# Performance work log

Measured on AMD Instinct MI355X. Metric: run time of the kernel, lower is better.

The kernel has to match this reference:

```python
import jax, jax.numpy as jnp
import numpy as np

B, T, N, D = 4, 128, 512, 32
CHEB_K, EMB, HEADS, TA_LAYERS, GCN_NUM, TCN_BLOCKS, KSIZE = 3, 10, 2, 2, 3, 3, 3


def setup_inputs() -> dict:
    key = jax.random.key(0)
    ks = jax.random.split(key, 12)
    x = jax.random.normal(ks[0], (B, T, N, D), jnp.float32)
    init_state = jnp.zeros((1, B, N, D), jnp.float32)  # unused by forward, kept for signature fidelity
    node_embeddings = jax.random.normal(ks[1], (N, EMB), jnp.float32)
    a = jax.random.uniform(ks[2], (N, N), jnp.float32)
    a = 0.5 * (a + a.T)
    adj = a / jnp.sum(a, axis=1, keepdims=True)  # row-normalized dense adjacency
    s = 0.05
    gcn_w = jax.random.normal(ks[3], (GCN_NUM, EMB, CHEB_K, D, D), jnp.float32) * s
    gcn_b = jax.random.normal(ks[4], (GCN_NUM, EMB, D), jnp.float32) * s
    tcn_w1 = jax.random.normal(ks[5], (TCN_BLOCKS, D, D, KSIZE), jnp.float32) * s
    tcn_b1 = jnp.zeros((TCN_BLOCKS, D), jnp.float32)
    tcn_w2 = jax.random.normal(ks[6], (TCN_BLOCKS, D, D, KSIZE), jnp.float32) * s
    tcn_b2 = jnp.zeros((TCN_BLOCKS, D), jnp.float32)
    ta_wq = jax.random.normal(ks[7], (TA_LAYERS, D, D), jnp.float32) * s
    ta_wk = jax.random.normal(ks[8], (TA_LAYERS, D, D), jnp.float32) * s
    ta_wv = jax.random.normal(ks[9], (TA_LAYERS, D, D), jnp.float32) * s
    ta_wo = jax.random.normal(ks[10], (TA_LAYERS, D, D), jnp.float32) * s
    ta_g = jnp.ones((TA_LAYERS, D), jnp.float32)
    ta_b = jnp.zeros((TA_LAYERS, D), jnp.float32)
    return dict(x=x, init_state=init_state, node_embeddings=node_embeddings, adj=adj,
                gcn_w=gcn_w, gcn_b=gcn_b, tcn_w1=tcn_w1, tcn_b1=tcn_b1, tcn_w2=tcn_w2,
                tcn_b2=tcn_b2, ta_wq=ta_wq, ta_wk=ta_wk, ta_wv=ta_wv, ta_wo=ta_wo,
                ta_g=ta_g, ta_b=ta_b)


def _cheb_supports(adj, k):
    I = jnp.eye(adj.shape[0], dtype=adj.dtype)
    s = [I, adj]
    for _ in range(2, k):
        s.append(2.0 * (adj @ s[-1]) - s[-2])
    return jnp.stack(s[:k])  # (k, N, N)


def _emb_gcn(h, supports, E, wp, bp):
    # h: (B,T,N,C); supports: (k,N,N); E: (N,EMB); wp: (EMB,k,C,O); bp: (EMB,O)
    xg = jnp.einsum('knm,btmc->btknc', supports, h)
    W = jnp.einsum('ne,ekco->nkco', E, wp)       # per-node Chebyshev weights
    bias = E @ bp                                 # (N,O)
    return jnp.einsum('btknc,nkco->btno', xg, W) + bias


def _causal_conv(y, w, b, dil):
    # y: (BN, C, T); w: (O, C, K)
    pad = (w.shape[-1] - 1) * dil
    out = jax.lax.conv_general_dilated(y, w, (1,), [(pad, 0)], rhs_dilation=(dil,),
                                       dimension_numbers=('NCH', 'OIH', 'NCH'))
    return out + b[None, :, None]


def _temporal_block(y, w1, b1, w2, b2, dil):
    o = jax.nn.relu(_causal_conv(y, w1, b1, dil))
    o = jax.nn.relu(_causal_conv(o, w2, b2, dil))
    return jax.nn.relu(o + y)  # residual (in_ch == out_ch)


def _layernorm(h, g, b):
    mu = jnp.mean(h, -1, keepdims=True)
    var = jnp.var(h, -1, keepdims=True)
    return (h - mu) * jax.lax.rsqrt(var + 1e-5) * g + b


def _attn_layer(h, wq, wk, wv, wo, g, b):
    # h: (BN, T, D) temporal self-attention
    bn, t, d = h.shape
    dh = d // HEADS
    scale = 1.0 / float(np.sqrt(dh))
    q = (h @ wq).reshape(bn, t, HEADS, dh)
    k = (h @ wk).reshape(bn, t, HEADS, dh)
    v = (h @ wv).reshape(bn, t, HEADS, dh)
    a = jax.nn.softmax(jnp.einsum('bqhd,bkhd->bhqk', q, k) * scale, axis=-1)
    o = jnp.einsum('bhqk,bkhd->bqhd', a, v).reshape(bn, t, d) @ wo
    return _layernorm(h + o, g, b)


def reference(x, init_state, node_embeddings, adj, gcn_w, gcn_b, tcn_w1, tcn_b1,
              tcn_w2, tcn_b2, ta_wq, ta_wk, ta_wv, ta_wo, ta_g, ta_b):
    supports = _cheb_supports(adj, CHEB_K)
    h = x
    for i in range(GCN_NUM):  # 3 stacked EmbGCN layers, vectorized over time
        h = _emb_gcn(h, supports, node_embeddings, gcn_w[i], gcn_b[i])
    b, t, n, d = h.shape
    y = jnp.transpose(h, (0, 2, 3, 1)).reshape(b * n, d, t)  # (BN, D, T)
    for i in range(TCN_BLOCKS):  # dilations 1,2,4
        y = _temporal_block(y, tcn_w1[i], tcn_b1[i], tcn_w2[i], tcn_b2[i], 2 ** i)
    h2 = jnp.transpose(y.reshape(b, n, d, t), (0, 1, 3, 2)).reshape(b * n, t, d)
    for i in range(TA_LAYERS):
        h2 = _attn_layer(h2, ta_wq[i], ta_wk[i], ta_wv[i], ta_wo[i], ta_g[i], ta_b[i])
    return jnp.transpose(h2.reshape(b, n, t, d), (0, 2, 1, 3))  # (B,T,N,D)
```

## Files before the change

### kernel.cpp

```cpp
#include <hip/hip_runtime.h>
#include <hip/hip_bf16.h>


typedef __attribute__((ext_vector_type(8))) short short8;
typedef __attribute__((ext_vector_type(4))) short short4v;
typedef __attribute__((ext_vector_type(4))) float float4v;

#define MFMA32(a, b, c) __builtin_amdgcn_mfma_f32_16x16x32_bf16((a), (b), (c), 0, 0, 0)
#if defined(__has_builtin)
#if __has_builtin(__builtin_amdgcn_mfma_f32_16x16x16_bf16)
#define MFMA16A(a, b, c) __builtin_amdgcn_mfma_f32_16x16x16_bf16((a), (b), (c), 0, 0, 0)
#endif
#endif
#ifndef MFMA16A
#define MFMA16A(a, b, c) __builtin_amdgcn_mfma_f32_16x16x16bf16_1k((a), (b), (c), 0, 0, 0)
#endif

#if defined(__has_builtin)
#if __has_builtin(__builtin_amdgcn_exp2f)
#define EXP2F(x) __builtin_amdgcn_exp2f(x)
#endif
#endif
#ifndef EXP2F
#define EXP2F(x) exp2f(x)
#endif

typedef const __attribute__((address_space(1))) unsigned int* gas_ptr;
typedef __attribute__((address_space(3))) unsigned int* las_ptr;
__device__ __forceinline__ void glds16(const void* g, void* l) {
  __builtin_amdgcn_global_load_lds((gas_ptr)g, (las_ptr)l, 16, 0, 0);
}

__device__ __forceinline__ unsigned int f2b2(float lo, float hi) {
  union { __hip_bfloat162 h; unsigned int u; } cv;
  cv.h = __float22bfloat162_rn(make_float2(lo, hi));
  return cv.u;
}
__device__ __forceinline__ unsigned short f2b(float f) {
  return (unsigned short)f2b2(f, f);
}
__device__ __forceinline__ float b2f(unsigned short u) {
  return __uint_as_float(((unsigned int)u) << 16);
}
__device__ __forceinline__ ushort4 f2b4(float a, float b, float c, float d) {
  union { unsigned int u[2]; ushort4 s; } cv;
  cv.u[0] = f2b2(a, b);
  cv.u[1] = f2b2(c, d);
  return cv.s;
}

__global__ void __launch_bounds__(256) prep_all(
    const float* __restrict__ adj, unsigned short* __restrict__ Sb,
    const float* __restrict__ emb, const float* __restrict__ gw,
    const float* __restrict__ gb, unsigned short* __restrict__ W8,
    float* __restrict__ biasn,
    const float* __restrict__ w1g, const float* __restrict__ w2g,
    unsigned short* __restrict__ Wt,
    const float* __restrict__ wqg, const float* __restrict__ wkg,
    const float* __restrict__ wvg, const float* __restrict__ wog,
    unsigned short* __restrict__ Wf,
    const float* __restrict__ x, unsigned short* __restrict__ H8,
    unsigned short* __restrict__ Hrm) {
  __shared__ unsigned short Asq[128 * 40];
  __shared__ unsigned short Bsq[128 * 40];
  int bid = blockIdx.x, tid = threadIdx.x;

  if (bid < 64) {
    int base = bid * 4096;
#pragma unroll
    for (int it = 0; it < 4; ++it) {
      int e = base + it * 1024 + tid * 4;
      float4 v = *(const float4*)&adj[e];
      union { unsigned int u[2]; ushort4 s; } pk;
      pk.u[0] = f2b2(v.x, v.y);
      pk.u[1] = f2b2(v.z, v.w);
      *(ushort4*)&Sb[e] = pk.s;
    }
    return;
  }
  if (bid < 80) {
    int tb = bid - 64;
    int mt = tb >> 2, jt = tb & 3;
    int m0 = mt * 128, j0 = jt * 128;
    int wave = tid >> 6, lane = tid & 63;
    int wm = wave >> 1, wj = wave & 1;
    int l15 = lane & 15, quad = lane >> 4;
    float4v acc[4][4];
#pragma unroll
    for (int a = 0; a < 4; ++a)
#pragma unroll
      for (int b = 0; b < 4; ++b) acc[a][b] = (float4v)0.f;
    for (int kt = 0; kt < 512; kt += 32) {
#pragma unroll
      for (int p = 0; p < 16; ++p) {
        int idx = p * 256 + tid;
        int m = idx >> 5, k = idx & 31;
        Asq[m * 40 + k] = f2b(adj[(m0 + m) * 512 + kt + k]);
      }
#pragma unroll
      for (int p = 0; p < 16; ++p) {
        int idx = p * 256 + tid;
        int k = idx >> 7, j = idx & 127;
        Bsq[j * 40 + k] = f2b(adj[(kt + k) * 512 + j0 + j]);
      }
      __syncthreads();
      short8 af[4], bfr[4];
#pragma unroll
      for (int mi = 0; mi < 4; ++mi)
        af[mi] = *(const short8*)&Asq[(wm * 64 + mi * 16 + l15) * 40 + quad * 8];
#pragma unroll
      for (int ji = 0; ji < 4; ++ji)
        bfr[ji] = *(const short8*)&Bsq[(wj * 64 + ji * 16 + l15) * 40 + quad * 8];
#pragma unroll
      for (int mi = 0; mi < 4; ++mi)
#pragma unroll
        for (int ji = 0; ji < 4; ++ji)
          acc[mi][ji] = MFMA32(af[mi], bfr[ji], acc[mi][ji]);
      __syncthreads();
    }
#pragma unroll
    for (int mi = 0; mi < 4; ++mi)
#pragma unroll
      for (int ji = 0; ji < 4; ++ji) {
        int j = j0 + wj * 64 + ji * 16 + l15;
#pragma unroll
        for (int r = 0; r < 4; ++r) {
          int m = m0 + wm * 64 + mi * 16 + quad * 4 + r;
          Sb[(512 + m) * 512 + j] =
              f2b(2.f * acc[mi][ji][r] - (m == j ? 1.f : 0.f));
        }
      }
    return;
  }
  if (bid < 1616) {
    int b2 = bid - 80;
    int i = b2 >> 9, n = b2 & 511;
    float ev[10];
#pragma unroll
    for (int e = 0; e < 10; ++e) ev[e] = emb[n * 10 + e];
    for (int idx = tid; idx < 3072; idx += 256) {
      int s = idx >> 10, c = (idx >> 5) & 31, o = idx & 31;
      float acc = 0.f;
#pragma unroll
      for (int e = 0; e < 10; ++e) acc += ev[e] * gw[(i * 10 + e) * 3072 + idx];
      W8[((i * 512 + n) * 3 + s) * 1024 + (c >> 3) * 256 + o * 8 + (c & 7)] =
          f2b(acc);
    }
    if (tid < 32) {
      float acc = 0.f;
#pragma unroll
      for (int e = 0; e < 10; ++e) acc += ev[e] * gb[(i * 10 + e) * 32 + tid];
      biasn[(i * 512 + n) * 32 + tid] = acc;
    }
    return;
  }
  if (bid < 1622) {
    int b2 = bid - 1616;
    int blk = b2 >> 1, conv = b2 & 1;
    const float* w = (conv ? w2g : w1g) + blk * 3072;
    for (int idx = tid; idx < 3072; idx += 256) {
      int kk = idx >> 10, rem = idx & 1023;
      int o = rem >> 5, c = rem & 31;
      Wt[b2 * 3072 + idx] = f2b(w[o * 96 + c * 3 + kk]);
    }
    return;
  }
  if (bid < 1654) {
    int idx = (bid - 1622) * 256 + tid;
    int L = idx >> 12;
    int mat = (idx >> 10) & 3;
    int nt = (idx >> 9) & 1;
    int lane = (idx >> 3) & 63;
    int j = idx & 7;
    int quad = lane >> 4, l15 = lane & 15;
    const float* base =
        (mat == 0 ? wqg : mat == 1 ? wkg : mat == 2 ? wvg : wog) + L * 1024;
    float v = base[(quad * 8 + j) * 32 + nt * 16 + l15];
    if (mat == 0) v *= 0.36067376022224085f;
    Wf[idx] = f2b(v);
    return;
  }
  {
    int b2 = bid - 1654;
    int nblk = b2 >> 3, part = b2 & 7;
    for (int qq = tid; qq < 2048; qq += 256) {
      int q = part * 2048 + qq;
      int bt = q >> 5, c = q & 31;
      const float* xb = x + bt * 16384 + nblk * 256 + c;
      float f[8];
#pragma unroll
      for (int s = 0; s < 8; ++s) f[s] = xb[s * 32];
      union { unsigned int u[4]; uint4 v; } pk;
      pk.u[0] = f2b2(f[0], f[1]);
      pk.u[1] = f2b2(f[2], f[3]);
      pk.u[2] = f2b2(f[4], f[5]);
      pk.u[3] = f2b2(f[6], f[7]);
      *(uint4*)&H8[nblk * 131072 + q * 8] = pk.v;
    }
    for (int qq = tid; qq < 2048; qq += 256) {
      int q = part * 2048 + qq;
      int s = q >> 11, e0 = (q & 2047) * 8;
      int bt = e0 >> 5, c0 = e0 & 31;
      const float* xb = x + bt * 16384 + (nblk * 8 + s) * 32 + c0;
      float4 v0 = *(const float4*)&xb[0];
      float4 v1 = *(const float4*)&xb[4];
      union { unsigned int u[4]; uint4 v; } pk;
      pk.u[0] = f2b2(v0.x, v0.y);
      pk.u[1] = f2b2(v0.z, v0.w);
      pk.u[2] = f2b2(v1.x, v1.y);
      pk.u[3] = f2b2(v1.z, v1.w);
      *(uint4*)&Hrm[(nblk * 8 + s) * 16384 + e0] = pk.v;
    }
  }
}

__global__ void __launch_bounds__(256) gcn_phaseA(
    const unsigned short* __restrict__ Sb,
    const unsigned short* __restrict__ H8,
    unsigned short* __restrict__ G) {
  __shared__ unsigned short As[2][128 * 32];
  __shared__ unsigned short Bs[2][4096];
  int bid0 = blockIdx.x;
  int nb = (bid0 & 7) * 128 + (bid0 >> 3);
  int mt = nb & 7, jt = nb >> 3;
  int m0 = mt * 128, j0 = jt * 128;
  int tid = threadIdx.x;
  int wave = tid >> 6, lane = tid & 63;
  int wm = wave >> 1, wj = wave & 1;
  int l15 = lane & 15, quad = lane >> 4;
  float4v acc[4][4];
#pragma unroll
  for (int a = 0; a < 4; ++a)
#pragma unroll
    for (int b = 0; b < 4; ++b) acc[a][b] = (float4v)0.f;
#pragma unroll
  for (int p = 0; p < 2; ++p) {
    int q = tid + p * 256;
    int m = q >> 2;
    int c8 = (q & 3) ^ ((q >> 3) & 3);
    glds16(&Sb[(m0 + m) * 512 + c8 * 8], &As[0][q * 8]);
  }
  {
    const unsigned short* hb = H8 + j0 * 8;
#pragma unroll
    for (int p = 0; p < 2; ++p) {
      int q = tid + p * 256;
      glds16(&hb[(q >> 7) * 131072 + (q & 127) * 8], &Bs[0][q * 8]);
    }
  }
  __syncthreads();
#pragma unroll 2
  for (int it = 0; it < 16; ++it) {
    int cur = it & 1;
    if (it < 15) {
      int ncn = (it + 1) * 32;
#pragma unroll
      for (int p = 0; p < 2; ++p) {
        int q = tid + p * 256;
        int m = q >> 2;
        int c8 = (q & 3) ^ ((q >> 3) & 3);
        glds16(&Sb[(m0 + m) * 512 + ncn + c8 * 8], &As[cur ^ 1][q * 8]);
      }
      const unsigned short* hb = H8 + (ncn >> 3) * 131072 + j0 * 8;
#pragma unroll
      for (int p = 0; p < 2; ++p) {
        int q = tid + p * 256;
        glds16(&hb[(q >> 7) * 131072 + (q & 127) * 8], &Bs[cur ^ 1][q * 8]);
      }
    }
    short8 af[4], bfr[4];
#pragma unroll
    for (int mi = 0; mi < 4; ++mi) {
      int row = wm * 64 + mi * 16 + l15;
      int c8 = quad ^ ((row >> 1) & 3);
      af[mi] = *(const short8*)&As[cur][row * 32 + c8 * 8];
    }
#pragma unroll
    for (int ji = 0; ji < 4; ++ji)
      bfr[ji] =
          *(const short8*)&Bs[cur][quad * 1024 + (wj * 64 + ji * 16 + l15) * 8];
#pragma unroll
    for (int mi = 0; mi < 4; ++mi)
#pragma unroll
      for (int ji = 0; ji < 4; ++ji)
        acc[mi][ji] = MFMA32(af[mi], bfr[ji], acc[mi][ji]);
    __syncthreads();
  }
#pragma unroll
  for (int mi = 0; mi < 4; ++mi)
#pragma unroll
    for (int ji = 0; ji < 4; ++ji) {
      int j = j0 + wj * 64 + ji * 16 + l15;
#pragma unroll
      for (int r = 0; r < 4; ++r) {
        int m = m0 + wm * 64 + mi * 16 + quad * 4 + r;
        G[m * 16384 + j] = f2b(acc[mi][ji][r]);
      }
    }
}

__global__ void __launch_bounds__(256) gcn_phaseB(
    const unsigned short* __restrict__ Hrm, const unsigned short* __restrict__ G,
    const unsigned short* __restrict__ W8, const float* __restrict__ biasn,
    unsigned short* __restrict__ H8out, unsigned short* __restrict__ Hrmout,
    unsigned short* __restrict__ tcnout) {
  int bid = blockIdx.x;
  int n = bid >> 1, bh = bid & 1;
  int tid = threadIdx.x;
  int lane = tid & 63, wave = tid >> 6, l15 = lane & 15, quad = lane >> 4;
  short8 wb[3][2];
#pragma unroll
  for (int s = 0; s < 3; ++s)
#pragma unroll
    for (int nt = 0; nt < 2; ++nt)
      wb[s][nt] = *(const short8*)&W8[(n * 3 + s) * 1024 + quad * 256 +
                                      (nt * 16 + l15) * 8];
  float b0 = biasn[n * 32 + l15], b1 = biasn[n * 32 + 16 + l15];
  int n8base = (n >> 3) * 131072 + (n & 7);
#pragma unroll
  for (int mi = 0; mi < 4; ++mi) {
    int bt0 = bh * 256 + wave * 64 + mi * 16;
    int btl = bt0 + l15;
    short8 a0 = *(const short8*)&Hrm[n * 16384 + btl * 32 + quad * 8];
    short8 a1 = *(const short8*)&G[n * 16384 + btl * 32 + quad * 8];
    short8 a2 = *(const short8*)&G[(512 + n) * 16384 + btl * 32 + quad * 8];
    float4v acc0 = MFMA32(a0, wb[0][0], (float4v)0.f);
    acc0 = MFMA32(a1, wb[1][0], acc0);
    acc0 = MFMA32(a2, wb[2][0], acc0);
    float4v acc1 = MFMA32(a0, wb[0][1], (float4v)0.f);
    acc1 = MFMA32(a1, wb[1][1], acc1);
    acc1 = MFMA32(a2, wb[2][1], acc1);
#pragma unroll
    for (int r = 0; r < 4; ++r) {
      int bt = bt0 + quad * 4 + r;
      unsigned short v0 = f2b(acc0[r] + b0);
      unsigned short v1 = f2b(acc1[r] + b1);
      if (tcnout) {
        int bb = bt >> 7, t = bt & 127;
        int o0 = l15, o1 = 16 + l15;
        tcnout[n * 16384 + bb * 4096 + (o0 >> 3) * 1024 + t * 8 + (o0 & 7)] = v0;
        tcnout[n * 16384 + bb * 4096 + (o1 >> 3) * 1024 + t * 8 + (o1 & 7)] = v1;
      } else {
        H8out[n8base + (bt * 32 + l15) * 8] = v0;
        H8out[n8base + (bt * 32 + 16 + l15) * 8] = v1;
        Hrmout[n * 16384 + bt * 32 + l15] = v0;
        Hrmout[n * 16384 + bt * 32 + 16 + l15] = v1;
      }
    }
  }
}

__global__ void __launch_bounds__(256) tcn_kernel(
    const unsigned short* __restrict__ Yin, unsigned short* __restrict__ yout,
    const unsigned short* __restrict__ Wt,
    const float* __restrict__ b1g, const float* __restrict__ b2g) {
  __shared__ unsigned short Y8[4][4352];
  __shared__ unsigned short O8[4][4352];
  int tid = threadIdx.x, wave = tid >> 6, lane = tid & 63;
  int l15 = lane & 15, quad = lane >> 4;
  int n = blockIdx.x, b = wave;
  unsigned short* y8 = &Y8[wave][0];
  unsigned short* o8 = &O8[wave][0];
  {
    int cg = lane >> 4, t = (lane >> 1) & 7, half = lane & 1;
    ushort4 z = {0, 0, 0, 0};
    *(ushort4*)&y8[(cg * 136 + t) * 8 + half * 4] = z;
    *(ushort4*)&o8[(cg * 136 + t) * 8 + half * 4] = z;
  }
  const unsigned short* src = Yin + n * 16384 + b * 4096;
#pragma unroll
  for (int p = 0; p < 8; ++p) {
    int e = p * 64 + lane;
    int cg = e >> 7, t = e & 127;
    *(uint4*)&y8[(cg * 136 + t + 8) * 8] = *(const uint4*)&src[e * 8];
  }
  for (int blk = 0; blk < 3; ++blk) {
    int dil = 1 << blk;
    for (int conv = 0; conv < 2; ++conv) {
      const unsigned short* wbase = Wt + ((blk * 2 + conv) * 3) * 1024;
      short8 af[2][3];
#pragma unroll
      for (int mt = 0; mt < 2; ++mt)
#pragma unroll
        for (int kk = 0; kk < 3; ++kk)
          af[mt][kk] = *(const short8*)&wbase[kk * 1024 +
                                              (mt * 16 + l15) * 32 + quad * 8];
      const float* bias = (conv ? b2g : b1g) + blk * 32;
      float4 bs0 = *(const float4*)&bias[quad * 4];
      float4 bs1 = *(const float4*)&bias[16 + quad * 4];
      float bb0[4] = {bs0.x, bs0.y, bs0.z, bs0.w};
      float bb1[4] = {bs1.x, bs1.y, bs1.z, bs1.w};
      const unsigned short* rbuf = conv ? o8 : y8;
#pragma unroll 2
      for (int nt = 0; nt < 8; ++nt) {
        float4v acc0 = (float4v)0.f, acc1 = (float4v)0.f;
#pragma unroll
        for (int kk = 0; kk < 3; ++kk) {
          int tb = nt * 16 + l15 + 8 - (2 - kk) * dil;
          short8 bf = *(const short8*)&rbuf[(quad * 136 + tb) * 8];
          acc0 = MFMA32(af[0][kk], bf, acc0);
          acc1 = MFMA32(af[1][kk], bf, acc1);
        }
        int t8 = nt * 16 + l15 + 8;
        int og0 = (quad >> 1), ci0 = (quad & 1) * 4;
        if (conv == 0) {
          ushort4 w0 = f2b4(fmaxf(acc0[0] + bb0[0], 0.f),
                            fmaxf(acc0[1] + bb0[1], 0.f),
                            fmaxf(acc0[2] + bb0[2], 0.f),
                            fmaxf(acc0[3] + bb0[3], 0.f));
          ushort4 w1 = f2b4(fmaxf(acc1[0] + bb1[0], 0.f),
                            fmaxf(acc1[1] + bb1[1], 0.f),
                            fmaxf(acc1[2] + bb1[2], 0.f),
                            fmaxf(acc1[3] + bb1[3], 0.f));
          *(ushort4*)&o8[((og0)*136 + t8) * 8 + ci0] = w0;
          *(ushort4*)&o8[((2 + og0) * 136 + t8) * 8 + ci0] = w1;
        } else {
          ushort4 y0 = *(const ushort4*)&y8[((og0)*136 + t8) * 8 + ci0];
          ushort4 y1 = *(const ushort4*)&y8[((2 + og0) * 136 + t8) * 8 + ci0];
          ushort4 w0 = f2b4(
              fmaxf(fmaxf(acc0[0] + bb0[0], 0.f) + b2f(y0.x), 0.f),
              fmaxf(fmaxf(acc0[1] + bb0[1], 0.f) + b2f(y0.y), 0.f),
              fmaxf(fmaxf(acc0[2] + bb0[2], 0.f) + b2f(y0.z), 0.f),
              fmaxf(fmaxf(acc0[3] + bb0[3], 0.f) + b2f(y0.w), 0.f));
          ushort4 w1 = f2b4(
              fmaxf(fmaxf(acc1[0] + bb1[0], 0.f) + b2f(y1.x), 0.f),
              fmaxf(fmaxf(acc1[1] + bb1[1], 0.f) + b2f(y1.y), 0.f),
              fmaxf(fmaxf(acc1[2] + bb1[2], 0.f) + b2f(y1.z), 0.f),
              fmaxf(fmaxf(acc1[3] + bb1[3], 0.f) + b2f(y1.w), 0.f));
          *(ushort4*)&y8[((og0)*136 + t8) * 8 + ci0] = w0;
          *(ushort4*)&y8[((2 + og0) * 136 + t8) * 8 + ci0] = w1;
        }
      }
    }
  }
  unsigned short* dst = yout + n * 16384 + b * 4096;
#pragma unroll
  for (int p = 0; p < 8; ++p) {
    int e = p * 64 + lane;
    int og = e >> 7, t = e & 127;
    *(uint4*)&dst[t * 32 + og * 8] = *(const uint4*)&y8[(og * 136 + t + 8) * 8];
  }
}

__global__ void __launch_bounds__(256) attn_kernel(
    const unsigned short* __restrict__ yin,
    float* __restrict__ outp,
    const unsigned short* __restrict__ Wf,
    const float* __restrict__ gg, const float* __restrict__ bgb) {
  __shared__ unsigned short hfrag[4096];
  __shared__ unsigned short KbOb[5120];
  __shared__ unsigned short QT[32 * 136];
  __shared__ unsigned short VT[32 * 136];
  int bn = blockIdx.x, tid = threadIdx.x;
  int b = bn >> 9, n = bn & 511;
  int lane = tid & 63, wave = tid >> 6;
  int l15 = lane & 15, quad = lane >> 4;
  int mt0 = wave * 2;

  const unsigned short* src = yin + n * 16384 + b * 4096;
  for (int q = tid; q < 512; q += 256) {
    int t = ((q >> 6) << 4) | (q & 15);
    int cb = (q >> 4) & 3;
    glds16(&src[(t * 4 + cb) * 8], &hfrag[q * 8]);
  }

  for (int L = 0; L < 2; ++L) {
    short8 wf[4][2];
#pragma unroll
    for (int mat = 0; mat < 4; ++mat)
#pragma unroll
      for (int nt = 0; nt < 2; ++nt)
        wf[mat][nt] =
            *(const short8*)&Wf[(((L * 4 + mat) * 2 + nt) * 64 + lane) * 8];
    __syncthreads();
#pragma unroll
    for (int mm = 0; mm < 2; ++mm) {
      int mtq = mt0 + mm;
      short8 af = *(const short8*)&hfrag[(mtq * 4 + quad) * 128 + l15 * 8];
      int tbase = mtq * 16 + quad * 4;
#pragma unroll
      for (int nt = 0; nt < 2; ++nt) {
        float4v qa = MFMA32(af, wf[0][nt], (float4v)0.f);
        float4v ka = MFMA32(af, wf[1][nt], (float4v)0.f);
        float4v va = MFMA32(af, wf[2][nt], (float4v)0.f);
        int d = nt * 16 + l15;
#pragma unroll
        for (int r = 0; r < 4; ++r) KbOb[(tbase + r) * 36 + d] = f2b(ka[r]);
        *(ushort4*)&QT[d * 136 + tbase] = f2b4(qa[0], qa[1], qa[2], qa[3]);
        *(ushort4*)&VT[d * 136 + tbase] = f2b4(va[0], va[1], va[2], va[3]);
      }
    }
    __syncthreads();
    float4v oaccT[2][2];
#pragma unroll
    for (int mm = 0; mm < 2; ++mm)
#pragma unroll
      for (int hh = 0; hh < 2; ++hh) oaccT[mm][hh] = (float4v)0.f;
    for (int hh = 0; hh < 2; ++hh) {
#pragma unroll
      for (int mm = 0; mm < 2; ++mm) {
        int mtq = mt0 + mm;
        short4v qb;
#pragma unroll
        for (int jj = 0; jj < 4; ++jj)
          qb[jj] = (short)QT[(hh * 16 + quad * 4 + jj) * 136 + mtq * 16 + l15];
        float4v sacc[8];
#pragma unroll
        for (int st = 0; st < 8; ++st) {
          short4v ka = *(const short4v*)&KbOb[(st * 16 + l15) * 36 + hh * 16 +
                                              quad * 4];
          sacc[st] = MFMA16A(ka, qb, (float4v)0.f);
        }
        float tmx[8];
#pragma unroll
        for (int st = 0; st < 8; ++st)
          tmx[st] = fmaxf(fmaxf(sacc[st][0], sacc[st][1]),
                          fmaxf(sacc[st][2], sacc[st][3]));
        float mx = fmaxf(fmaxf(fmaxf(tmx[0], tmx[1]), fmaxf(tmx[2], tmx[3])),
                         fmaxf(fmaxf(tmx[4], tmx[5]), fmaxf(tmx[6], tmx[7])));
        mx = fmaxf(mx, __shfl_xor(mx, 16));
        mx = fmaxf(mx, __shfl_xor(mx, 32));
        float ps[8];
#pragma unroll
        for (int st = 0; st < 8; ++st) {
#pragma unroll
          for (int r = 0; r < 4; ++r) sacc[st][r] = EXP2F(sacc[st][r] - mx);
          ps[st] = (sacc[st][0] + sacc[st][1]) + (sacc[st][2] + sacc[st][3]);
        }
        float sum = ((ps[0] + ps[1]) + (ps[2] + ps[3])) +
                    ((ps[4] + ps[5]) + (ps[6] + ps[7]));
        sum += __shfl_xor(sum, 16);
        sum += __shfl_xor(sum, 32);
        float inv = 1.f / sum;
#pragma unroll
        for (int st = 0; st < 8; ++st) {
          union { unsigned int u[2]; short4v s; } pv;
          pv.u[0] = f2b2(sacc[st][0], sacc[st][1]);
          pv.u[1] = f2b2(sacc[st][2], sacc[st][3]);
          short4v va = *(const short4v*)&VT[(hh * 16 + l15) * 136 + st * 16 +
                                            quad * 4];
          oaccT[mm][hh] = MFMA16A(va, pv.s, oaccT[mm][hh]);
        }
#pragma unroll
        for (int r = 0; r < 4; ++r) oaccT[mm][hh][r] *= inv;
      }
    }
    __syncthreads();
#pragma unroll
    for (int mm = 0; mm < 2; ++mm) {
      int mtq = mt0 + mm;
#pragma unroll
      for (int hh = 0; hh < 2; ++hh)
        *(ushort4*)&KbOb[(mtq * 16 + l15) * 40 + hh * 16 + quad * 4] =
            f2b4(oaccT[mm][hh][0], oaccT[mm][hh][1], oaccT[mm][hh][2],
                 oaccT[mm][hh][3]);
    }
    float gam0 = gg[L * 32 + l15], bet0 = bgb[L * 32 + l15];
    float gam1 = gg[L * 32 + 16 + l15], bet1 = bgb[L * 32 + 16 + l15];
#pragma unroll
    for (int mm = 0; mm < 2; ++mm) {
      int mtq = mt0 + mm;
      short8 ofa = *(const short8*)&KbOb[(mtq * 16 + l15) * 40 + quad * 8];
      float4v racc0 = MFMA32(ofa, wf[3][0], (float4v)0.f);
      float4v racc1 = MFMA32(ofa, wf[3][1], (float4v)0.f);
      int hi0 = (mtq * 4 + (l15 >> 3)) * 128 + (l15 & 7);
      int hi1 = (mtq * 4 + 2 + (l15 >> 3)) * 128 + (l15 & 7);
#pragma unroll
      for (int r = 0; r < 4; ++r) {
        int t = mtq * 16 + quad * 4 + r;
        int ro = (quad * 4 + r) * 8;
        float v0 = racc0[r] + b2f(hfrag[hi0 + ro]);
        float v1 = racc1[r] + b2f(hfrag[hi1 + ro]);
        float s = v0 + v1;
        for (int m = 1; m < 16; m <<= 1) s += __shfl_xor(s, m);
        float mu = s * 0.03125f;
        float d0 = v0 - mu, d1 = v1 - mu;
        float q = d0 * d0 + d1 * d1;
        for (int m = 1; m < 16; m <<= 1) q += __shfl_xor(q, m);
        float rs = rsqrtf(q * 0.03125f + 1e-5f);
        float y0 = d0 * rs * gam0 + bet0;
        float y1 = d1 * rs * gam1 + bet1;
        if (L == 0) {
          hfrag[hi0 + ro] = f2b(y0);
          hfrag[hi1 + ro] = f2b(y1);
        } else {
          outp[((b * 128 + t) * 512 + n) * 32 + l15] = y0;
          outp[((b * 128 + t) * 512 + n) * 32 + 16 + l15] = y1;
        }
      }
    }
  }
}

extern "C" void kernel_launch(void* const* d_in, const int* in_sizes, int n_in,
                              void* d_out, int out_size, void* d_ws, size_t ws_size,
                              hipStream_t stream) {
  const float* x    = (const float*)d_in[0];
  const float* emb  = (const float*)d_in[2];
  const float* adj  = (const float*)d_in[3];
  const float* gw   = (const float*)d_in[4];
  const float* gb   = (const float*)d_in[5];
  const float* tw1  = (const float*)d_in[6];
  const float* tb1  = (const float*)d_in[7];
  const float* tw2  = (const float*)d_in[8];
  const float* tb2  = (const float*)d_in[9];
  const float* wq   = (const float*)d_in[10];
  const float* wk   = (const float*)d_in[11];
  const float* wv   = (const float*)d_in[12];
  const float* wo   = (const float*)d_in[13];
  const float* tg   = (const float*)d_in[14];
  const float* tbb  = (const float*)d_in[15];
  float* outp = (float*)d_out;

  char* p = (char*)d_ws;
  unsigned short* Sb  = (unsigned short*)p; p += 1048576;
  unsigned short* W8  = (unsigned short*)p; p += 9437184;
  float* biasn        = (float*)p;          p += 196608;
  unsigned short* G   = (unsigned short*)p; p += 33554432;
  unsigned short* H8a = (unsigned short*)p; p += 16777216;
  unsigned short* H8b = (unsigned short*)p; p += 16777216;
  unsigned short* Hra = (unsigned short*)p; p += 16777216;
  unsigned short* Hrb = (unsigned short*)p; p += 16777216;
  unsigned short* Wt  = (unsigned short*)p; p += 36864;
  unsigned short* Wf  = (unsigned short*)p; p += 16384;

  prep_all<<<dim3(2166), dim3(256), 0, stream>>>(
      adj, Sb, emb, gw, gb, W8, biasn, tw1, tw2, Wt, wq, wk, wv, wo, Wf,
      x, H8a, Hra);

  gcn_phaseA<<<dim3(1024), dim3(256), 0, stream>>>(Sb, H8a, G);
  gcn_phaseB<<<dim3(1024), dim3(256), 0, stream>>>(
      Hra, G, W8, biasn, H8b, Hrb, (unsigned short*)nullptr);
  gcn_phaseA<<<dim3(1024), dim3(256), 0, stream>>>(Sb, H8b, G);
  gcn_phaseB<<<dim3(1024), dim3(256), 0, stream>>>(
      Hrb, G, W8 + 1572864, biasn + 16384, H8a, Hra, (unsigned short*)nullptr);
  gcn_phaseA<<<dim3(1024), dim3(256), 0, stream>>>(Sb, H8a, G);
  gcn_phaseB<<<dim3(1024), dim3(256), 0, stream>>>(
      Hra, G, W8 + 3145728, biasn + 32768, (unsigned short*)nullptr,
      (unsigned short*)nullptr, H8b);

  tcn_kernel<<<dim3(512), dim3(256), 0, stream>>>(H8b, H8a, Wt, tb1, tb2);
  attn_kernel<<<dim3(2048), dim3(256), 0, stream>>>(H8a, outp, Wf, tg, tbb);
}
```

Baseline: 384.9 us.

## Use 256-row GCN tiles and 512-thread blocks for GCN phaseA and attention

gcn_phaseA now uses 512-thread blocks with a 256-row tile of the support matrix. Each staged H8 tile is therefore reused across twice as many rows, and the grid shrinks to half as many blocks. attn_kernel now gives each of 8 waves a single 16-row time tile, instead of 4 waves handling two tiles each, which adds in-block parallelism. The costs are higher LDS use and register pressure per GCN block, fewer GCN blocks to spread over the CUs, and removal of the unroll-2 hint on the main loop.

```diff
diff --git a/kernel.cpp b/kernel.cpp
--- a/kernel.cpp
+++ b/kernel.cpp
@@ -214,16 +214,16 @@
   }
 }
 
-__global__ void __launch_bounds__(256) gcn_phaseA(
+__global__ void __launch_bounds__(512) gcn_phaseA(
     const unsigned short* __restrict__ Sb,
     const unsigned short* __restrict__ H8,
     unsigned short* __restrict__ G) {
-  __shared__ unsigned short As[2][128 * 32];
+  __shared__ unsigned short As[2][256 * 32];
   __shared__ unsigned short Bs[2][4096];
   int bid0 = blockIdx.x;
-  int nb = (bid0 & 7) * 128 + (bid0 >> 3);
-  int mt = nb & 7, jt = nb >> 3;
-  int m0 = mt * 128, j0 = jt * 128;
+  int nb = (bid0 & 7) * 64 + (bid0 >> 3);
+  int mt = nb & 3, jt = nb >> 2;
+  int m0 = mt * 256, j0 = jt * 128;
   int tid = threadIdx.x;
   int wave = tid >> 6, lane = tid & 63;
   int wm = wave >> 1, wj = wave & 1;
@@ -235,38 +235,26 @@
     for (int b = 0; b < 4; ++b) acc[a][b] = (float4v)0.f;
 #pragma unroll
   for (int p = 0; p < 2; ++p) {
-    int q = tid + p * 256;
+    int q = tid + p * 512;
     int m = q >> 2;
     int c8 = (q & 3) ^ ((q >> 3) & 3);
     glds16(&Sb[(m0 + m) * 512 + c8 * 8], &As[0][q * 8]);
   }
-  {
-    const unsigned short* hb = H8 + j0 * 8;
-#pragma unroll
-    for (int p = 0; p < 2; ++p) {
-      int q = tid + p * 256;
-      glds16(&hb[(q >> 7) * 131072 + (q & 127) * 8], &Bs[0][q * 8]);
-    }
-  }
+  glds16(&H8[(tid >> 7) * 131072 + (j0 + (tid & 127)) * 8], &Bs[0][tid * 8]);
   __syncthreads();
-#pragma unroll 2
   for (int it = 0; it < 16; ++it) {
     int cur = it & 1;
     if (it < 15) {
       int ncn = (it + 1) * 32;
 #pragma unroll
       for (int p = 0; p < 2; ++p) {
-        int q = tid + p * 256;
+        int q = tid + p * 512;
         int m = q >> 2;
         int c8 = (q & 3) ^ ((q >> 3) & 3);
         glds16(&Sb[(m0 + m) * 512 + ncn + c8 * 8], &As[cur ^ 1][q * 8]);
       }
-      const unsigned short* hb = H8 + (ncn >> 3) * 131072 + j0 * 8;
-#pragma unroll
-      for (int p = 0; p < 2; ++p) {
-        int q = tid + p * 256;
-        glds16(&hb[(q >> 7) * 131072 + (q & 127) * 8], &Bs[cur ^ 1][q * 8]);
-      }
+      glds16(&H8[((ncn >> 3) + (tid >> 7)) * 131072 + (j0 + (tid & 127)) * 8],
+             &Bs[cur ^ 1][tid * 8]);
     }
     short8 af[4], bfr[4];
 #pragma unroll
@@ -442,7 +430,7 @@
   }
 }
 
-__global__ void __launch_bounds__(256) attn_kernel(
+__global__ void __launch_bounds__(512) attn_kernel(
     const unsigned short* __restrict__ yin,
     float* __restrict__ outp,
     const unsigned short* __restrict__ Wf,
@@ -455,13 +443,13 @@
   int b = bn >> 9, n = bn & 511;
   int lane = tid & 63, wave = tid >> 6;
   int l15 = lane & 15, quad = lane >> 4;
-  int mt0 = wave * 2;
-
-  const unsigned short* src = yin + n * 16384 + b * 4096;
-  for (int q = tid; q < 512; q += 256) {
+  int mtq = wave;
+
+  {
+    int q = tid;
     int t = ((q >> 6) << 4) | (q & 15);
     int cb = (q >> 4) & 3;
-    glds16(&src[(t * 4 + cb) * 8], &hfrag[q * 8]);
+    glds16(&yin[n * 16384 + b * 4096 + (t * 4 + cb) * 8], &hfrag[q * 8]);
   }
 
   for (int L = 0; L < 2; ++L) {
@@ -473,9 +461,7 @@
         wf[mat][nt] =
             *(const short8*)&Wf[(((L * 4 + mat) * 2 + nt) * 64 + lane) * 8];
     __syncthreads();
-#pragma unroll
-    for (int mm = 0; mm < 2; ++mm) {
-      int mtq = mt0 + mm;
+    {
       short8 af = *(const short8*)&hfrag[(mtq * 4 + quad) * 128 + l15 * 8];
       int tbase = mtq * 16 + quad * 4;
 #pragma unroll
@@ -491,75 +477,62 @@
       }
     }
     __syncthreads();
-    float4v oaccT[2][2];
-#pragma unroll
-    for (int mm = 0; mm < 2; ++mm)
-#pragma unroll
-      for (int hh = 0; hh < 2; ++hh) oaccT[mm][hh] = (float4v)0.f;
+    float4v oaccT[2];
+#pragma unroll
+    for (int hh = 0; hh < 2; ++hh) oaccT[hh] = (float4v)0.f;
     for (int hh = 0; hh < 2; ++hh) {
-#pragma unroll
-      for (int mm = 0; mm < 2; ++mm) {
-        int mtq = mt0 + mm;
-        short4v qb;
-#pragma unroll
-        for (int jj = 0; jj < 4; ++jj)
-          qb[jj] = (short)QT[(hh * 16 + quad * 4 + jj) * 136 + mtq * 16 + l15];
-        float4v sacc[8];
-#pragma unroll
-        for (int st = 0; st < 8; ++st) {
-          short4v ka = *(const short4v*)&KbOb[(st * 16 + l15) * 36 + hh * 16 +
-                                              quad * 4];
-          sacc[st] = MFMA16A(ka, qb, (float4v)0.f);
-        }
-        float tmx[8];
-#pragma unroll
-        for (int st = 0; st < 8; ++st)
-          tmx[st] = fmaxf(fmaxf(sacc[st][0], sacc[st][1]),
-                          fmaxf(sacc[st][2], sacc[st][3]));
-        float mx = fmaxf(fmaxf(fmaxf(tmx[0], tmx[1]), fmaxf(tmx[2], tmx[3])),
-                         fmaxf(fmaxf(tmx[4], tmx[5]), fmaxf(tmx[6], tmx[7])));
-        mx = fmaxf(mx, __shfl_xor(mx, 16));
-        mx = fmaxf(mx, __shfl_xor(mx, 32));
-        float ps[8];
-#pragma unroll
-        for (int st = 0; st < 8; ++st) {
-#pragma unroll
-          for (int r = 0; r < 4; ++r) sacc[st][r] = EXP2F(sacc[st][r] - mx);
-          ps[st] = (sacc[st][0] + sacc[st][1]) + (sacc[st][2] + sacc[st][3]);
-        }
-        float sum = ((ps[0] + ps[1]) + (ps[2] + ps[3])) +
-                    ((ps[4] + ps[5]) + (ps[6] + ps[7]));
-        sum += __shfl_xor(sum, 16);
-        sum += __shfl_xor(sum, 32);
-        float inv = 1.f / sum;
-#pragma unroll
-        for (int st = 0; st < 8; ++st) {
-          union { unsigned int u[2]; short4v s; } pv;
-          pv.u[0] = f2b2(sacc[st][0], sacc[st][1]);
-          pv.u[1] = f2b2(sacc[st][2], sacc[st][3]);
-          short4v va = *(const short4v*)&VT[(hh * 16 + l15) * 136 + st * 16 +
+      short4v qb;
+#pragma unroll
+      for (int jj = 0; jj < 4; ++jj)
+        qb[jj] = (short)QT[(hh * 16 + quad * 4 + jj) * 136 + mtq * 16 + l15];
+      float4v sacc[8];
+#pragma unroll
+      for (int st = 0; st < 8; ++st) {
+        short4v ka = *(const short4v*)&KbOb[(st * 16 + l15) * 36 + hh * 16 +
                                             quad * 4];
-          oaccT[mm][hh] = MFMA16A(va, pv.s, oaccT[mm][hh]);
-        }
-#pragma unroll
-        for (int r = 0; r < 4; ++r) oaccT[mm][hh][r] *= inv;
-      }
+        sacc[st] = MFMA16A(ka, qb, (float4v)0.f);
+      }
+      float tmx[8];
+#pragma unroll
+      for (int st = 0; st < 8; ++st)
+        tmx[st] = fmaxf(fmaxf(sacc[st][0], sacc[st][1]),
+                        fmaxf(sacc[st][2], sacc[st][3]));
+      float mx = fmaxf(fmaxf(fmaxf(tmx[0], tmx[1]), fmaxf(tmx[2], tmx[3])),
+                       fmaxf(fmaxf(tmx[4], tmx[5]), fmaxf(tmx[6], tmx[7])));
+      mx = fmaxf(mx, __shfl_xor(mx, 16));
+      mx = fmaxf(mx, __shfl_xor(mx, 32));
+      float ps[8];
+#pragma unroll
+      for (int st = 0; st < 8; ++st) {
+#pragma unroll
+        for (int r = 0; r < 4; ++r) sacc[st][r] = EXP2F(sacc[st][r] - mx);
+        ps[st] = (sacc[st][0] + sacc[st][1]) + (sacc[st][2] + sacc[st][3]);
+      }
+      float sum = ((ps[0] + ps[1]) + (ps[2] + ps[3])) +
+                  ((ps[4] + ps[5]) + (ps[6] + ps[7]));
+      sum += __shfl_xor(sum, 16);
+      sum += __shfl_xor(sum, 32);
+      float inv = 1.f / sum;
+#pragma unroll
+      for (int st = 0; st < 8; ++st) {
+        union { unsigned int u[2]; short4v s; } pv;
+        pv.u[0] = f2b2(sacc[st][0], sacc[st][1]);
+        pv.u[1] = f2b2(sacc[st][2], sacc[st][3]);
+        short4v va = *(const short4v*)&VT[(hh * 16 + l15) * 136 + st * 16 +
+                                          quad * 4];
+        oaccT[hh] = MFMA16A(va, pv.s, oaccT[hh]);
+      }
+#pragma unroll
+      for (int r = 0; r < 4; ++r) oaccT[hh][r] *= inv;
     }
     __syncthreads();
 #pragma unroll
-    for (int mm = 0; mm < 2; ++mm) {
-      int mtq = mt0 + mm;
-#pragma unroll
-      for (int hh = 0; hh < 2; ++hh)
-        *(ushort4*)&KbOb[(mtq * 16 + l15) * 40 + hh * 16 + quad * 4] =
-            f2b4(oaccT[mm][hh][0], oaccT[mm][hh][1], oaccT[mm][hh][2],
-                 oaccT[mm][hh][3]);
-    }
+    for (int hh = 0; hh < 2; ++hh)
+      *(ushort4*)&KbOb[(mtq * 16 + l15) * 40 + hh * 16 + quad * 4] =
+          f2b4(oaccT[hh][0], oaccT[hh][1], oaccT[hh][2], oaccT[hh][3]);
     float gam0 = gg[L * 32 + l15], bet0 = bgb[L * 32 + l15];
     float gam1 = gg[L * 32 + 16 + l15], bet1 = bgb[L * 32 + 16 + l15];
-#pragma unroll
-    for (int mm = 0; mm < 2; ++mm) {
-      int mtq = mt0 + mm;
+    {
       short8 ofa = *(const short8*)&KbOb[(mtq * 16 + l15) * 40 + quad * 8];
       float4v racc0 = MFMA32(ofa, wf[3][0], (float4v)0.f);
       float4v racc1 = MFMA32(ofa, wf[3][1], (float4v)0.f);
@@ -628,17 +601,17 @@
       adj, Sb, emb, gw, gb, W8, biasn, tw1, tw2, Wt, wq, wk, wv, wo, Wf,
       x, H8a, Hra);
 
-  gcn_phaseA<<<dim3(1024), dim3(256), 0, stream>>>(Sb, H8a, G);
+  gcn_phaseA<<<dim3(512), dim3(512), 0, stream>>>(Sb, H8a, G);
   gcn_phaseB<<<dim3(1024), dim3(256), 0, stream>>>(
       Hra, G, W8, biasn, H8b, Hrb, (unsigned short*)nullptr);
-  gcn_phaseA<<<dim3(1024), dim3(256), 0, stream>>>(Sb, H8b, G);
+  gcn_phaseA<<<dim3(512), dim3(512), 0, stream>>>(Sb, H8b, G);
   gcn_phaseB<<<dim3(1024), dim3(256), 0, stream>>>(
       Hrb, G, W8 + 1572864, biasn + 16384, H8a, Hra, (unsigned short*)nullptr);
-  gcn_phaseA<<<dim3(1024), dim3(256), 0, stream>>>(Sb, H8a, G);
+  gcn_phaseA<<<dim3(512), dim3(512), 0, stream>>>(Sb, H8a, G);
   gcn_phaseB<<<dim3(1024), dim3(256), 0, stream>>>(
       Hra, G, W8 + 3145728, biasn + 32768, (unsigned short*)nullptr,
       (unsigned short*)nullptr, H8b);
 
   tcn_kernel<<<dim3(512), dim3(256), 0, stream>>>(H8b, H8a, Wt, tb1, tb2);
-  attn_kernel<<<dim3(2048), dim3(256), 0, stream>>>(H8a, outp, Wf, tg, tbb);
-}
+  attn_kernel<<<dim3(2048), dim3(512), 0, stream>>>(H8a, outp, Wf, tg, tbb);
+}
```

Measured after the change: 346.9 us. 1.11x faster.
